# Kernel optimization log

Hardware: AMD Instinct MI355X
Metric: run time of the kernel (lower is better)

Reference implementation:

```python
import jax, jax.numpy as jnp
import numpy as np
import math

B, T, C, H = 8, 1024, 1024, 16
HS = C // H  # head size 64
FF = 4 * C
EPS = 1e-5


def quant_weight(W, e, b):
    """Fake-quant with straight-through rounding, per QLinear.forward.
    W:[...,out,in], e:[...,out,1], b:[...,out,1] -> effective weight 2**e * round_ste(clip(2**-e * W))."""
    b_rel = jax.nn.relu(b)
    mn = jnp.where(b_rel > 0, -(2.0 ** (b_rel - 1)), 0.0)
    mx = jnp.where(b_rel > 0, 2.0 ** (b_rel - 1) - 1.0, 0.0)
    qw = jnp.clip((2.0 ** (-e)) * W, mn, mx)
    w = qw + jax.lax.stop_gradient(jnp.round(qw) - qw)  # STE round
    return (2.0 ** e) * w


def layer_norm(x, g, beta):
    mu = jnp.mean(x, axis=-1, keepdims=True)
    var = jnp.mean((x - mu) ** 2, axis=-1, keepdims=True)
    return (x - mu) * jax.lax.rsqrt(var + EPS) * g + beta


def _uniform(key, shape, fan_in):
    s = 1.0 / math.sqrt(fan_in)
    return jax.random.uniform(key, shape, jnp.float32, -s, s)


def setup_inputs() -> dict:
    key = jax.random.key(0)
    ks = jax.random.split(key, 8)
    d = {"x": jax.random.normal(ks[0], (B, T, C), jnp.float32)}
    # stacked per-head QKV QLinear params (bias=False)
    d["Wq"] = _uniform(ks[1], (H, HS, C), C)
    d["Wk"] = _uniform(ks[2], (H, HS, C), C)
    d["Wv"] = _uniform(ks[3], (H, HS, C), C)
    for n in ("q", "k", "v"):
        d["e" + n] = jnp.full((H, HS, 1), -8.0, jnp.float32)
        d["b" + n] = jnp.full((H, HS, 1), 32.0, jnp.float32)
    # output projection QLinear (bias=True)
    d["Wp"] = _uniform(ks[4], (C, C), C)
    d["ep"] = jnp.full((C, 1), -8.0, jnp.float32)
    d["bp"] = jnp.full((C, 1), 32.0, jnp.float32)
    d["biasp"] = jnp.zeros((C,), jnp.float32)
    # FFN QLinears
    d["W1"] = _uniform(ks[5], (FF, C), C)
    d["e1"] = jnp.full((FF, 1), -8.0, jnp.float32)
    d["b1"] = jnp.full((FF, 1), 32.0, jnp.float32)
    d["bias1"] = jnp.zeros((FF,), jnp.float32)
    d["W2"] = _uniform(ks[6], (C, FF), FF)
    d["e2"] = jnp.full((C, 1), -8.0, jnp.float32)
    d["b2"] = jnp.full((C, 1), 32.0, jnp.float32)
    d["bias2"] = jnp.zeros((C,), jnp.float32)
    # LayerNorms
    d["g1"] = jnp.ones((C,), jnp.float32)
    d["be1"] = jnp.zeros((C,), jnp.float32)
    d["g2"] = jnp.ones((C,), jnp.float32)
    d["be2"] = jnp.zeros((C,), jnp.float32)
    return d


def block_forward(x, Wq, eq, bq, Wk, ek, bk, Wv, ev, bv,
                  Wp, ep, bp, biasp, W1, e1, b1, bias1, W2, e2, b2, bias2,
                  g1, be1, g2, be2):
    h = layer_norm(x, g1, be1)
    q = jnp.einsum('btc,hdc->bhtd', h, quant_weight(Wq, eq, bq))
    k = jnp.einsum('btc,hdc->bhtd', h, quant_weight(Wk, ek, bk))
    v = jnp.einsum('btc,hdc->bhtd', h, quant_weight(Wv, ev, bv))
    # NOTE: source scales by C**-0.5 where C = n_embd (not head_size)
    wei = jnp.einsum('bhtd,bhsd->bhts', q, k) * (C ** -0.5)
    causal = jnp.tril(jnp.ones((T, T), bool))
    wei = jnp.where(causal, wei, -jnp.inf)
    wei = jax.nn.softmax(wei, axis=-1)
    att = jnp.einsum('bhts,bhsd->bhtd', wei, v)  # [B,H,T,HS]
    att = att.transpose(0, 2, 1, 3).reshape(B, T, C)  # concat heads
    x = x + att @ quant_weight(Wp, ep, bp).T + biasp
    h2 = layer_norm(x, g2, be2)
    f = jax.nn.relu(h2 @ quant_weight(W1, e1, b1).T + bias1)
    f = f @ quant_weight(W2, e2, b2).T + bias2
    return x + f


def reference(x, Wq, eq, bq, Wk, ek, bk, Wv, ev, bv,
              Wp, ep, bp, biasp, W1, e1, b1, bias1, W2, e2, b2, bias2,
              g1, be1, g2, be2):
    return block_forward(x, Wq, eq, bq, Wk, ek, bk, Wv, ev, bv,
                         Wp, ep, bp, biasp, W1, e1, b1, bias1, W2, e2, b2, bias2,
                         g1, be1, g2, be2)
```

## Files before the change

kernel.cpp:

```cpp
#include <hip/hip_runtime.h>
#include <hip/hip_bf16.h>
#include <math.h>

#define DEVI __device__ __forceinline__

typedef __attribute__((ext_vector_type(8))) short bf16x8;
typedef __attribute__((ext_vector_type(4))) float f32x4;

DEVI unsigned short f2bf(float f) {
    union { float f; unsigned u; } v; v.f = f;
    unsigned r = v.u + 0x7FFFu + ((v.u >> 16) & 1u);
    return (unsigned short)(r >> 16);
}

DEVI void gload16(const void* g, void* l) {
    __builtin_amdgcn_global_load_lds((const __attribute__((address_space(1))) void*)g,
                                     (__attribute__((address_space(3))) void*)l, 16, 0, 0);
}

#define WAITVM8() asm volatile("s_waitcnt vmcnt(8)" ::: "memory")
#define WAITVM4() asm volatile("s_waitcnt vmcnt(4)" ::: "memory")
#define WAITVM0() asm volatile("s_waitcnt vmcnt(0)" ::: "memory")
#define WAITLG0() asm volatile("s_waitcnt lgkmcnt(0)" ::: "memory")
#define WAITLG8() asm volatile("s_waitcnt lgkmcnt(8)" ::: "memory")
#define BAR()     __builtin_amdgcn_s_barrier()
#define SB()      __builtin_amdgcn_sched_barrier(0)

__global__ __launch_bounds__(256) void quant6_kernel(
    const float* __restrict__ Wq, const float* __restrict__ Wk, const float* __restrict__ Wv,
    const float* __restrict__ Wp, const float* __restrict__ W1, const float* __restrict__ W2,
    const float* __restrict__ eq, const float* __restrict__ ek, const float* __restrict__ ev,
    const float* __restrict__ ep, const float* __restrict__ e1, const float* __restrict__ e2,
    const float* __restrict__ bq, const float* __restrict__ bk, const float* __restrict__ bv,
    const float* __restrict__ bp, const float* __restrict__ b1, const float* __restrict__ b2,
    unsigned short* __restrict__ Wqkvq, unsigned short* __restrict__ Wpq,
    unsigned short* __restrict__ W1q, unsigned short* __restrict__ W2q)
{
    const int M1 = 1 << 20;
    const int NCH = 3 * M1;
    for (int c = blockIdx.x * blockDim.x + threadIdx.x; c < NCH; c += gridDim.x * blockDim.x) {
        int elem = c * 4;
        const float *W, *e, *b; unsigned short* o; int lgK, local;
        if (elem < M1)            { W = Wq; e = eq; b = bq; o = Wqkvq;          lgK = 10; local = elem; }
        else if (elem < 2 * M1)   { W = Wk; e = ek; b = bk; o = Wqkvq + M1;     lgK = 10; local = elem - M1; }
        else if (elem < 3 * M1)   { W = Wv; e = ev; b = bv; o = Wqkvq + 2 * M1; lgK = 10; local = elem - 2 * M1; }
        else if (elem < 4 * M1)   { W = Wp; e = ep; b = bp; o = Wpq;            lgK = 10; local = elem - 3 * M1; }
        else if (elem < 8 * M1)   { W = W1; e = e1; b = b1; o = W1q;            lgK = 10; local = elem - 4 * M1; }
        else                      { W = W2; e = e2; b = b2; o = W2q;            lgK = 12; local = elem - 8 * M1; }
        int row = local >> lgK;
        float evv = e[row], bvv = b[row];
        float br = fmaxf(bvv, 0.f);
        float mn, mx;
        if (br > 0.f) { float p = exp2f(br - 1.f); mn = -p; mx = p - 1.f; }
        else          { mn = 0.f; mx = 0.f; }
        float si = exp2f(-evv), so = exp2f(evv);
        union { float4 v4; float a[4]; } v;
        v.v4 = *(const float4*)(W + local);
        union { unsigned short u[4]; unsigned long long ll; } ot;
        #pragma unroll
        for (int j = 0; j < 4; j++) {
            float qw = fminf(fmaxf(si * v.a[j], mn), mx);
            ot.u[j] = f2bf(so * rintf(qw));
        }
        *(unsigned long long*)(o + local) = ot.ll;
    }
}

__global__ __launch_bounds__(256) void ln_kernel(
    const float* __restrict__ x, const float* __restrict__ g, const float* __restrict__ be,
    unsigned short* __restrict__ out)
{
    int row = blockIdx.x;
    union { float4 v4; float a[4]; } v;
    v.v4 = ((const float4*)(x + (size_t)row * 1024))[threadIdx.x];
    float s = v.a[0] + v.a[1] + v.a[2] + v.a[3];
    float s2 = v.a[0]*v.a[0] + v.a[1]*v.a[1] + v.a[2]*v.a[2] + v.a[3]*v.a[3];
    #pragma unroll
    for (int off = 32; off > 0; off >>= 1) { s += __shfl_down(s, off); s2 += __shfl_down(s2, off); }
    __shared__ float ps[4], ps2[4];
    int wave = threadIdx.x >> 6, lane = threadIdx.x & 63;
    if (lane == 0) { ps[wave] = s; ps2[wave] = s2; }
    __syncthreads();
    float mu = (ps[0] + ps[1] + ps[2] + ps[3]) * (1.0f / 1024.0f);
    float var = (ps2[0] + ps2[1] + ps2[2] + ps2[3]) * (1.0f / 1024.0f) - mu * mu;
    float rs = rsqrtf(var + 1e-5f);
    int c = threadIdx.x * 4;
    union { unsigned short u[4]; unsigned long long ll; } o;
    #pragma unroll
    for (int j = 0; j < 4; j++) o.u[j] = f2bf((v.a[j] - mu) * rs * g[c + j] + be[c + j]);
    *(unsigned long long*)(out + (size_t)row * 1024 + c) = o.ll;
}

#define GSTAGE(buf, kt) do { \
    _Pragma("unroll") for (int q_ = 0; q_ < 4; q_++) { \
        int idx_ = q_ * 256 + tid; int row_ = idx_ >> 3; int gs_ = (idx_ & 7) ^ (row_ & 7); \
        gload16(A  + (size_t)(brow + row_) * K + (kt) * 64 + gs_ * 8, &As[buf][idx_ * 8]); \
        gload16(Bw + (size_t)(bcol + row_) * K + (kt) * 64 + gs_ * 8, &Bs[buf][idx_ * 8]); \
    } } while (0)

template<int EP>
__global__ __launch_bounds__(256) void gemm_bt(
    const unsigned short* __restrict__ A, const unsigned short* __restrict__ Bw,
    int N, int K,
    const float* __restrict__ bias, const float* __restrict__ res,
    float* __restrict__ outf, unsigned short* __restrict__ outb)
{
    __shared__ __align__(16) unsigned short As[2][128 * 64];
    __shared__ __align__(16) unsigned short Bs[2][128 * 64];
    int tid = threadIdx.x, lane = tid & 63, wave = tid >> 6;
    int gx = gridDim.x;
    int nwg = gx * gridDim.y;
    int id = blockIdx.y * gx + blockIdx.x;
    int swz = (id & 7) * (nwg >> 3) + (id >> 3);
    int brow = (swz / gx) * 128, bcol = (swz % gx) * 128;
    int wr = wave >> 1, wc = wave & 1;
    int r = lane & 15, g4 = lane >> 4;
    f32x4 acc[4][4];
    #pragma unroll
    for (int i = 0; i < 4; i++)
        #pragma unroll
        for (int j = 0; j < 4; j++) acc[i][j] = (f32x4){0.f, 0.f, 0.f, 0.f};

    int nt = K >> 6;
    GSTAGE(0, 0);
    __syncthreads();
    int cur = 0;
    for (int t = 0; t < nt; ++t) {
        if (t + 1 < nt) { GSTAGE(cur ^ 1, t + 1); WAITVM8(); }
        else            { WAITVM0(); }
        __builtin_amdgcn_s_barrier();
        #pragma unroll
        for (int kk = 0; kk < 2; kk++) {
            bf16x8 af[4], bfr[4];
            #pragma unroll
            for (int mi = 0; mi < 4; mi++) {
                int rh = wr * 64 + mi * 16 + r;
                af[mi] = *(const bf16x8*)&As[cur][rh * 64 + (((kk * 4 + g4) ^ (rh & 7)) << 3)];
            }
            #pragma unroll
            for (int ni = 0; ni < 4; ni++) {
                int rh = wc * 64 + ni * 16 + r;
                bfr[ni] = *(const bf16x8*)&Bs[cur][rh * 64 + (((kk * 4 + g4) ^ (rh & 7)) << 3)];
            }
            #pragma unroll
            for (int mi = 0; mi < 4; mi++)
                #pragma unroll
                for (int ni = 0; ni < 4; ni++)
                    acc[mi][ni] = __builtin_amdgcn_mfma_f32_16x16x32_bf16(af[mi], bfr[ni], acc[mi][ni], 0, 0, 0);
        }
        __builtin_amdgcn_s_barrier();
        cur ^= 1;
    }

    #pragma unroll
    for (int mi = 0; mi < 4; mi++)
        #pragma unroll
        for (int ni = 0; ni < 4; ni++)
            #pragma unroll
            for (int i = 0; i < 4; i++) {
                int row = brow + wr * 64 + mi * 16 + g4 * 4 + i;
                int col = bcol + wc * 64 + ni * 16 + r;
                float v = acc[mi][ni][i];
                if (EP == 0) {
                    outb[(size_t)row * N + col] = f2bf(v);
                } else if (EP == 1) {
                    outf[(size_t)row * N + col] = v + bias[col] + res[(size_t)row * N + col];
                } else {
                    outb[(size_t)row * N + col] = f2bf(fmaxf(v + bias[col], 0.f));
                }
            }
}

#define STAGE_A(b, h, kt) do { \
    _Pragma("unroll") \
    for (int ld = 0; ld < 2; ld++) { \
        int idx = ld * 512 + tid; int rw = idx >> 3; int gs = (idx & 7) ^ (rw & 7); \
        gload16(Aa + (size_t)(brow + (h) * 128 + rw) * K + (kt) * 64 + gs * 8, &As[b][h][idx * 8]); \
    } } while (0)

#define STAGE_B(b, h, kt) do { \
    _Pragma("unroll") \
    for (int ld = 0; ld < 2; ld++) { \
        int idx = ld * 512 + tid; int rw = idx >> 3; int gs = (idx & 7) ^ (rw & 7); \
        gload16(Bw + (size_t)(bcol + (h) * 128 + rw) * K + (kt) * 64 + gs * 8, &Bs[b][h][idx * 8]); \
    } } while (0)

#define RD_A(b, mh) do { \
    _Pragma("unroll") for (int mi = 0; mi < 4; mi++) \
    _Pragma("unroll") for (int kk = 0; kk < 2; kk++) { \
        int rh = (mh) * 64 + mi * 16 + r; \
        af[mi][kk] = *(const bf16x8*)&As[b][wr][rh * 64 + (((kk * 4 + g4) ^ (rh & 7)) << 3)]; \
    } } while (0)

#define RD_B2(b, nh) do { \
    _Pragma("unroll") for (int nj = 0; nj < 2; nj++) \
    _Pragma("unroll") for (int kk = 0; kk < 2; kk++) { \
        int rh = (wc & 1) * 64 + ((nh) * 2 + nj) * 16 + r; \
        bfr[(nh) * 2 + nj][kk] = *(const bf16x8*)&Bs[b][wc >> 1][rh * 64 + (((kk * 4 + g4) ^ (rh & 7)) << 3)]; \
    } } while (0)

#define QUAD(mh, nh) do { \
    __builtin_amdgcn_s_setprio(1); \
    _Pragma("unroll") for (int mi = 0; mi < 4; mi++) \
    _Pragma("unroll") for (int nj = 0; nj < 2; nj++) \
    _Pragma("unroll") for (int kk = 0; kk < 2; kk++) \
        acc[(mh) * 4 + mi][(nh) * 2 + nj] = __builtin_amdgcn_mfma_f32_16x16x32_bf16( \
            af[mi][kk], bfr[(nh) * 2 + nj][kk], acc[(mh) * 4 + mi][(nh) * 2 + nj], 0, 0, 0); \
    __builtin_amdgcn_s_setprio(0); \
    } while (0)

template<int EP>
__global__ __launch_bounds__(512, 2) void gemm256(
    const unsigned short* __restrict__ Aa, const unsigned short* __restrict__ Bw,
    int N, int K,
    const float* __restrict__ bias, const float* __restrict__ res,
    float* __restrict__ outf, unsigned short* __restrict__ outb)
{
    __shared__ __align__(16) unsigned short As[2][2][128 * 64];
    __shared__ __align__(16) unsigned short Bs[2][2][128 * 64];
    int tid = threadIdx.x, lane = tid & 63, wave = tid >> 6;
    int gx = gridDim.x;
    int nwg = gx * gridDim.y;
    int id = blockIdx.y * gx + blockIdx.x;
    int swz = (id & 7) * (nwg >> 3) + (id >> 3);
    int brow = (swz / gx) * 256, bcol = (swz % gx) * 256;
    int wr = wave >> 2, wc = wave & 3;
    int r = lane & 15, g4 = lane >> 4;
    int KT = K >> 6;

    f32x4 acc[8][4];
    #pragma unroll
    for (int i = 0; i < 8; i++)
        #pragma unroll
        for (int j = 0; j < 4; j++) acc[i][j] = (f32x4){0.f, 0.f, 0.f, 0.f};
    bf16x8 af[4][2], bfr[4][2];

    STAGE_A(0, 0, 0); STAGE_A(0, 1, 0); STAGE_B(0, 0, 0); STAGE_B(0, 1, 0);
    STAGE_B(1, 0, 1); STAGE_B(1, 1, 1);
    WAITVM4();
    BAR();

    for (int t = 0; t < KT; t += 2) {
        RD_A(0, 0); RD_B2(0, 0);
        STAGE_A(1, 0, t + 1);
        WAITLG8();
        BAR(); WAITLG0(); SB();
        QUAD(0, 0);
        BAR();
        RD_B2(0, 1);
        STAGE_A(1, 1, t + 1);
        BAR(); WAITLG0(); SB();
        QUAD(0, 1);
        BAR();
        RD_A(0, 1);
        if (t + 2 < KT) STAGE_B(0, 0, t + 2);
        BAR(); WAITLG0(); SB();
        QUAD(1, 1);
        BAR();
        if (t + 2 < KT) { STAGE_B(0, 1, t + 2); WAITVM4(); } else { WAITVM0(); }
        BAR(); WAITLG0(); SB();
        QUAD(1, 0);
        BAR();
        RD_A(1, 0); RD_B2(1, 0);
        if (t + 2 < KT) STAGE_A(0, 0, t + 2);
        WAITLG8();
        BAR(); WAITLG0(); SB();
        QUAD(0, 0);
        BAR();
        RD_B2(1, 1);
        if (t + 2 < KT) STAGE_A(0, 1, t + 2);
        BAR(); WAITLG0(); SB();
        QUAD(0, 1);
        BAR();
        RD_A(1, 1);
        if (t + 3 < KT) STAGE_B(1, 0, t + 3);
        BAR(); WAITLG0(); SB();
        QUAD(1, 1);
        BAR();
        if (t + 3 < KT) { STAGE_B(1, 1, t + 3); WAITVM4(); } else { WAITVM0(); }
        BAR(); WAITLG0(); SB();
        QUAD(1, 0);
        BAR();
    }

    #pragma unroll
    for (int m = 0; m < 8; m++)
        #pragma unroll
        for (int n = 0; n < 4; n++)
            #pragma unroll
            for (int j = 0; j < 4; j++) {
                int row = brow + wr * 128 + m * 16 + g4 * 4 + j;
                int col = bcol + wc * 64 + n * 16 + r;
                float v = acc[m][n][j];
                if (EP == 0) {
                    outb[(size_t)row * N + col] = f2bf(v);
                } else if (EP == 1) {
                    outf[(size_t)row * N + col] = v + bias[col] + res[(size_t)row * N + col];
                } else {
                    outb[(size_t)row * N + col] = f2bf(fmaxf(v + bias[col], 0.f));
                }
            }
}

__global__ __launch_bounds__(256) void attn_kernel(
    const unsigned short* __restrict__ qkv, unsigned short* __restrict__ att)
{
    __shared__ __align__(16) unsigned short Ks[2][64 * 64];
    __shared__ __align__(16) unsigned short Vt[2][64 * 64];
    __shared__ __align__(16) unsigned short Ps[64 * 64];
    int tid = threadIdx.x, lane = tid & 63, wave = tid >> 6;
    int pi = blockIdx.x;
    int bh = blockIdx.y, bb = bh >> 4, hh = bh & 15;
    int r = lane & 15, g4 = lane >> 4;
    const unsigned short* base = qkv + (size_t)bb * 1024 * 3072;
    const float SCL = 0.03125f * 1.4426950408889634f;
    int vd = tid & 63, vsb = tid >> 6;
    int prow = wave * 16 + r;
    int pswz = (r & 7) << 3;

    #pragma unroll
    for (int sub = 0; sub < 2; sub++) {
        int qi = sub ? (15 - pi) : pi;
        int q0 = qi * 64;
        int qrow = q0 + prow;

        bf16x8 qf[2];
        #pragma unroll
        for (int kk = 0; kk < 2; kk++)
            qf[kk] = *(const bf16x8*)&base[(size_t)qrow * 3072 + hh * 64 + kk * 32 + g4 * 8];

        f32x4 oacc[4];
        #pragma unroll
        for (int i = 0; i < 4; i++) oacc[i] = (f32x4){0.f, 0.f, 0.f, 0.f};
        float m_i = -INFINITY, l_i = 0.f;

        unsigned short vtmp[16];
        {
            #pragma unroll
            for (int half = 0; half < 2; half++) {
                int idx = half * 256 + tid;
                int row = idx >> 3, slot = idx & 7;
                int gs = slot ^ (row & 7);
                gload16(base + (size_t)row * 3072 + 1024 + hh * 64 + gs * 8, &Ks[0][idx * 8]);
            }
            #pragma unroll
            for (int i2 = 0; i2 < 16; i2++)
                vtmp[i2] = base[(size_t)(vsb * 16 + i2) * 3072 + 2048 + hh * 64 + vd];
            union { unsigned short u[8]; bf16x8 v; } w0, w1;
            #pragma unroll
            for (int i2 = 0; i2 < 8; i2++) { w0.u[i2] = vtmp[i2]; w1.u[i2] = vtmp[8 + i2]; }
            int s0 = (vsb * 2) ^ (vd & 7), s1 = (vsb * 2 + 1) ^ (vd & 7);
            *(bf16x8*)&Vt[0][vd * 64 + s0 * 8] = w0.v;
            *(bf16x8*)&Vt[0][vd * 64 + s1 * 8] = w1.v;
        }
        __syncthreads();

        for (int ki = 0; ki <= qi; ki++) {
            int cur = ki & 1;
            bool pre = (ki < qi);
            if (pre) {
                int k1 = (ki + 1) * 64;
                #pragma unroll
                for (int half = 0; half < 2; half++) {
                    int idx = half * 256 + tid;
                    int row = idx >> 3, slot = idx & 7;
                    int gs = slot ^ (row & 7);
                    gload16(base + (size_t)(k1 + row) * 3072 + 1024 + hh * 64 + gs * 8, &Ks[cur ^ 1][idx * 8]);
                }
                #pragma unroll
                for (int i2 = 0; i2 < 16; i2++)
                    vtmp[i2] = base[(size_t)(k1 + vsb * 16 + i2) * 3072 + 2048 + hh * 64 + vd];
            }

            int k0 = ki * 64;
            f32x4 sacc[4];
            #pragma unroll
            for (int c4 = 0; c4 < 4; c4++) sacc[c4] = (f32x4){0.f, 0.f, 0.f, 0.f};
            #pragma unroll
            for (int c4 = 0; c4 < 4; c4++) {
                int krow = c4 * 16 + r;
                #pragma unroll
                for (int kk = 0; kk < 2; kk++) {
                    int slot = (g4 + kk * 4) ^ (krow & 7);
                    bf16x8 kf = *(const bf16x8*)&Ks[cur][krow * 64 + slot * 8];
                    sacc[c4] = __builtin_amdgcn_mfma_f32_16x16x32_bf16(kf, qf[kk], sacc[c4], 0, 0, 0);
                }
            }
            bool diag = (ki == qi);
            float sv[4][4];
            float smax = -INFINITY;
            #pragma unroll
            for (int c4 = 0; c4 < 4; c4++)
                #pragma unroll
                for (int i = 0; i < 4; i++) {
                    float s = sacc[c4][i];
                    if (diag && (k0 + c4 * 16 + g4 * 4 + i) > qrow) s = -INFINITY;
                    sv[c4][i] = s;
                    smax = fmaxf(smax, s);
                }
            smax = fmaxf(smax, __shfl_xor(smax, 16));
            smax = fmaxf(smax, __shfl_xor(smax, 32));
            float mn = fmaxf(m_i, smax);
            float fs = exp2f((m_i - mn) * SCL);
            float nb = -mn * SCL;
            m_i = mn;
            float rsum = 0.f;
            float pv[4][4];
            #pragma unroll
            for (int c4 = 0; c4 < 4; c4++)
                #pragma unroll
                for (int i = 0; i < 4; i++) {
                    float p = exp2f(fmaf(sv[c4][i], SCL, nb));
                    pv[c4][i] = p;
                    rsum += p;
                }
            rsum += __shfl_xor(rsum, 16);
            rsum += __shfl_xor(rsum, 32);
            l_i = l_i * fs + rsum;
            #pragma unroll
            for (int n4 = 0; n4 < 4; n4++)
                #pragma unroll
                for (int i = 0; i < 4; i++) oacc[n4][i] *= fs;
            #pragma unroll
            for (int c4 = 0; c4 < 4; c4++) {
                union { unsigned short u[4]; unsigned long long ll; } pk;
                #pragma unroll
                for (int i = 0; i < 4; i++) pk.u[i] = f2bf(pv[c4][i]);
                int idx16 = (prow * 64 + c4 * 16 + g4 * 4) ^ pswz;
                *(unsigned long long*)&Ps[idx16] = pk.ll;
            }
            WAITLG0();
            if (pre) {
                union { unsigned short u[8]; bf16x8 v; } w0, w1;
                #pragma unroll
                for (int i2 = 0; i2 < 8; i2++) { w0.u[i2] = vtmp[i2]; w1.u[i2] = vtmp[8 + i2]; }
                int s0 = (vsb * 2) ^ (vd & 7), s1 = (vsb * 2 + 1) ^ (vd & 7);
                *(bf16x8*)&Vt[cur ^ 1][vd * 64 + s0 * 8] = w0.v;
                *(bf16x8*)&Vt[cur ^ 1][vd * 64 + s1 * 8] = w1.v;
            }
            bf16x8 pa[2];
            #pragma unroll
            for (int kk = 0; kk < 2; kk++)
                pa[kk] = *(const bf16x8*)&Ps[(prow * 64 + kk * 32 + g4 * 8) ^ pswz];
            #pragma unroll
            for (int n4 = 0; n4 < 4; n4++) {
                int d = n4 * 16 + r;
                #pragma unroll
                for (int kk = 0; kk < 2; kk++) {
                    bf16x8 vf = *(const bf16x8*)&Vt[cur][d * 64 + (((kk * 4 + g4) ^ (d & 7)) << 3)];
                    oacc[n4] = __builtin_amdgcn_mfma_f32_16x16x32_bf16(vf, pa[kk], oacc[n4], 0, 0, 0);
                }
            }
            __syncthreads();
        }

        float inv = 1.f / l_i;
        #pragma unroll
        for (int n4 = 0; n4 < 4; n4++) {
            union { unsigned short u[4]; unsigned long long ll; } ok;
            #pragma unroll
            for (int i = 0; i < 4; i++) ok.u[i] = f2bf(oacc[n4][i] * inv);
            size_t oidx = ((size_t)(bb * 1024 + qrow)) * 1024 + hh * 64 + n4 * 16 + g4 * 4;
            *(unsigned long long*)&att[oidx] = ok.ll;
        }
    }
}

extern "C" void kernel_launch(void* const* d_in, const int* in_sizes, int n_in,
                              void* d_out, int out_size, void* d_ws, size_t ws_size,
                              hipStream_t stream)
{
    const float* x     = (const float*)d_in[0];
    const float* Wq    = (const float*)d_in[1];
    const float* Wk    = (const float*)d_in[2];
    const float* Wv    = (const float*)d_in[3];
    const float* eq    = (const float*)d_in[4];
    const float* bq    = (const float*)d_in[5];
    const float* ek    = (const float*)d_in[6];
    const float* bk    = (const float*)d_in[7];
    const float* ev    = (const float*)d_in[8];
    const float* bv    = (const float*)d_in[9];
    const float* Wp    = (const float*)d_in[10];
    const float* ep    = (const float*)d_in[11];
    const float* bp    = (const float*)d_in[12];
    const float* biasp = (const float*)d_in[13];
    const float* W1    = (const float*)d_in[14];
    const float* e1    = (const float*)d_in[15];
    const float* b1    = (const float*)d_in[16];
    const float* bias1 = (const float*)d_in[17];
    const float* W2    = (const float*)d_in[18];
    const float* e2    = (const float*)d_in[19];
    const float* b2    = (const float*)d_in[20];
    const float* bias2 = (const float*)d_in[21];
    const float* g1    = (const float*)d_in[22];
    const float* be1   = (const float*)d_in[23];
    const float* g2    = (const float*)d_in[24];
    const float* be2   = (const float*)d_in[25];

    const size_t MB = 1ull << 20;
    char* ws = (char*)d_ws;
    unsigned short* Wqkvq = (unsigned short*)(ws);
    unsigned short* Wpq   = (unsigned short*)(ws + 6 * MB);
    unsigned short* W1q   = (unsigned short*)(ws + 8 * MB);
    unsigned short* W2q   = (unsigned short*)(ws + 16 * MB);
    unsigned short* hbuf  = (unsigned short*)(ws + 24 * MB);
    unsigned short* qkvb  = (unsigned short*)(ws + 40 * MB);
    unsigned short* fbuf  = qkvb;
    unsigned short* attb  = (unsigned short*)(ws + 88 * MB);
    float*          x2    = (float*)(ws + 104 * MB);

    quant6_kernel<<<2048, 256, 0, stream>>>(Wq, Wk, Wv, Wp, W1, W2,
                                            eq, ek, ev, ep, e1, e2,
                                            bq, bk, bv, bp, b1, b2,
                                            Wqkvq, Wpq, W1q, W2q);

    ln_kernel<<<8192, 256, 0, stream>>>(x, g1, be1, hbuf);
    gemm256<0><<<dim3(12, 32), 512, 0, stream>>>(hbuf, Wqkvq, 3072, 1024, nullptr, nullptr, nullptr, qkvb);
    attn_kernel<<<dim3(8, 128), 256, 0, stream>>>(qkvb, attb);
    gemm_bt<1><<<dim3(8, 64), 256, 0, stream>>>(attb, Wpq, 1024, 1024, biasp, x, x2, nullptr);
    ln_kernel<<<8192, 256, 0, stream>>>(x2, g2, be2, hbuf);
    gemm256<2><<<dim3(16, 32), 512, 0, stream>>>(hbuf, W1q, 4096, 1024, bias1, nullptr, nullptr, fbuf);
    gemm_bt<1><<<dim3(8, 64), 256, 0, stream>>>(fbuf, W2q, 1024, 4096, bias2, x2, (float*)d_out, nullptr);
}
```

Baseline: 349.5 us.

## Share K/V tiles across two query tiles per 512-thread attention block

The attention kernel now uses 512 threads, and each half of the block handles an adjacent query tile. Every K/V tile loaded into shared memory serves both query tiles, which halves global K/V traffic and staging per block. It also adds lazy online-softmax rescaling that only rescales when the row max grows by more than a threshold, packed bf16 conversion through v_cvt_pk_bf16_f32, and padding of the V-transpose LDS rows to a stride of 66. The costs are that the lower-tile waves sit idle on the last diagonal tile, and that the padded stride leaves 16-byte LDS accesses that are not 16-byte aligned.

```diff
diff --git a/kernel.cpp b/kernel.cpp
--- a/kernel.cpp
+++ b/kernel.cpp
@@ -11,6 +11,12 @@
     union { float f; unsigned u; } v; v.f = f;
     unsigned r = v.u + 0x7FFFu + ((v.u >> 16) & 1u);
     return (unsigned short)(r >> 16);
+}
+
+DEVI unsigned cvtpk(float lo, float hi) {
+    unsigned d;
+    asm volatile("v_cvt_pk_bf16_f32 %0, %1, %2" : "=v"(d) : "v"(lo), "v"(hi));
+    return d;
 }
 
 DEVI void gload16(const void* g, void* l) {
@@ -302,27 +308,28 @@
             }
 }
 
-__global__ __launch_bounds__(256) void attn_kernel(
+__global__ __launch_bounds__(512, 4) void attn_kernel(
     const unsigned short* __restrict__ qkv, unsigned short* __restrict__ att)
 {
     __shared__ __align__(16) unsigned short Ks[2][64 * 64];
-    __shared__ __align__(16) unsigned short Vt[2][64 * 64];
-    __shared__ __align__(16) unsigned short Ps[64 * 64];
-    int tid = threadIdx.x, lane = tid & 63, wave = tid >> 6;
+    __shared__ __align__(16) unsigned short Vt[2][64 * 66];
+    __shared__ __align__(16) unsigned short Ps[2][64 * 64];
+    int tid = threadIdx.x, lane = tid & 63, w = tid >> 6;
+    int half = w >> 2;
     int pi = blockIdx.x;
     int bh = blockIdx.y, bb = bh >> 4, hh = bh & 15;
     int r = lane & 15, g4 = lane >> 4;
     const unsigned short* base = qkv + (size_t)bb * 1024 * 3072;
     const float SCL = 0.03125f * 1.4426950408889634f;
     int vd = tid & 63, vsb = tid >> 6;
-    int prow = wave * 16 + r;
+    int prow = (w & 3) * 16 + r;
     int pswz = (r & 7) << 3;
 
-    #pragma unroll
-    for (int sub = 0; sub < 2; sub++) {
-        int qi = sub ? (15 - pi) : pi;
-        int q0 = qi * 64;
-        int qrow = q0 + prow;
+    for (int sidx = 0; sidx < 2; sidx++) {
+        int s = sidx ? (7 - pi) : pi;
+        int qt = 2 * s + half;
+        int qtmax = 2 * s + 1;
+        int qrow = qt * 64 + prow;
 
         bf16x8 qf[2];
         #pragma unroll
@@ -334,121 +341,115 @@
         for (int i = 0; i < 4; i++) oacc[i] = (f32x4){0.f, 0.f, 0.f, 0.f};
         float m_i = -INFINITY, l_i = 0.f;
 
-        unsigned short vtmp[16];
+        unsigned short vtmp[8];
         {
-            #pragma unroll
-            for (int half = 0; half < 2; half++) {
-                int idx = half * 256 + tid;
-                int row = idx >> 3, slot = idx & 7;
-                int gs = slot ^ (row & 7);
-                gload16(base + (size_t)row * 3072 + 1024 + hh * 64 + gs * 8, &Ks[0][idx * 8]);
-            }
-            #pragma unroll
-            for (int i2 = 0; i2 < 16; i2++)
-                vtmp[i2] = base[(size_t)(vsb * 16 + i2) * 3072 + 2048 + hh * 64 + vd];
-            union { unsigned short u[8]; bf16x8 v; } w0, w1;
-            #pragma unroll
-            for (int i2 = 0; i2 < 8; i2++) { w0.u[i2] = vtmp[i2]; w1.u[i2] = vtmp[8 + i2]; }
-            int s0 = (vsb * 2) ^ (vd & 7), s1 = (vsb * 2 + 1) ^ (vd & 7);
-            *(bf16x8*)&Vt[0][vd * 64 + s0 * 8] = w0.v;
-            *(bf16x8*)&Vt[0][vd * 64 + s1 * 8] = w1.v;
+            int row = tid >> 3, slot = tid & 7;
+            int gs = slot ^ (row & 7);
+            gload16(base + (size_t)row * 3072 + 1024 + hh * 64 + gs * 8, &Ks[0][tid * 8]);
+            #pragma unroll
+            for (int i2 = 0; i2 < 8; i2++)
+                vtmp[i2] = base[(size_t)(vsb * 8 + i2) * 3072 + 2048 + hh * 64 + vd];
+            union { unsigned short u[8]; bf16x8 v; } w0;
+            #pragma unroll
+            for (int i2 = 0; i2 < 8; i2++) w0.u[i2] = vtmp[i2];
+            *(bf16x8*)&Vt[0][vd * 66 + (vsb ^ (vd & 7)) * 8] = w0.v;
         }
         __syncthreads();
 
-        for (int ki = 0; ki <= qi; ki++) {
+        for (int ki = 0; ki <= qtmax; ki++) {
             int cur = ki & 1;
-            bool pre = (ki < qi);
+            bool pre = (ki < qtmax);
+            bool act = (ki <= qt);
             if (pre) {
                 int k1 = (ki + 1) * 64;
-                #pragma unroll
-                for (int half = 0; half < 2; half++) {
-                    int idx = half * 256 + tid;
-                    int row = idx >> 3, slot = idx & 7;
-                    int gs = slot ^ (row & 7);
-                    gload16(base + (size_t)(k1 + row) * 3072 + 1024 + hh * 64 + gs * 8, &Ks[cur ^ 1][idx * 8]);
+                int row = tid >> 3, slot = tid & 7;
+                int gs = slot ^ (row & 7);
+                gload16(base + (size_t)(k1 + row) * 3072 + 1024 + hh * 64 + gs * 8, &Ks[cur ^ 1][tid * 8]);
+                #pragma unroll
+                for (int i2 = 0; i2 < 8; i2++)
+                    vtmp[i2] = base[(size_t)(k1 + vsb * 8 + i2) * 3072 + 2048 + hh * 64 + vd];
+            }
+
+            if (act) {
+                int k0 = ki * 64;
+                f32x4 sacc[4];
+                #pragma unroll
+                for (int c4 = 0; c4 < 4; c4++) sacc[c4] = (f32x4){0.f, 0.f, 0.f, 0.f};
+                #pragma unroll
+                for (int c4 = 0; c4 < 4; c4++) {
+                    int krow = c4 * 16 + r;
+                    #pragma unroll
+                    for (int kk = 0; kk < 2; kk++) {
+                        int slot = (g4 + kk * 4) ^ (krow & 7);
+                        bf16x8 kf = *(const bf16x8*)&Ks[cur][krow * 64 + slot * 8];
+                        sacc[c4] = __builtin_amdgcn_mfma_f32_16x16x32_bf16(kf, qf[kk], sacc[c4], 0, 0, 0);
+                    }
                 }
-                #pragma unroll
-                for (int i2 = 0; i2 < 16; i2++)
-                    vtmp[i2] = base[(size_t)(k1 + vsb * 16 + i2) * 3072 + 2048 + hh * 64 + vd];
-            }
-
-            int k0 = ki * 64;
-            f32x4 sacc[4];
-            #pragma unroll
-            for (int c4 = 0; c4 < 4; c4++) sacc[c4] = (f32x4){0.f, 0.f, 0.f, 0.f};
-            #pragma unroll
-            for (int c4 = 0; c4 < 4; c4++) {
-                int krow = c4 * 16 + r;
-                #pragma unroll
-                for (int kk = 0; kk < 2; kk++) {
-                    int slot = (g4 + kk * 4) ^ (krow & 7);
-                    bf16x8 kf = *(const bf16x8*)&Ks[cur][krow * 64 + slot * 8];
-                    sacc[c4] = __builtin_amdgcn_mfma_f32_16x16x32_bf16(kf, qf[kk], sacc[c4], 0, 0, 0);
+                bool diag = (ki == qt);
+                float sv[4][4];
+                float smax = -INFINITY;
+                #pragma unroll
+                for (int c4 = 0; c4 < 4; c4++)
+                    #pragma unroll
+                    for (int i = 0; i < 4; i++) {
+                        float sa = sacc[c4][i];
+                        if (diag && (k0 + c4 * 16 + g4 * 4 + i) > qrow) sa = -INFINITY;
+                        sv[c4][i] = sa;
+                        smax = fmaxf(smax, sa);
+                    }
+                smax = fmaxf(smax, __shfl_xor(smax, 16));
+                smax = fmaxf(smax, __shfl_xor(smax, 32));
+                if (!__all((smax - m_i) * SCL <= 8.f)) {
+                    float mn = fmaxf(m_i, smax);
+                    float fs = exp2f((m_i - mn) * SCL);
+                    m_i = mn;
+                    l_i *= fs;
+                    #pragma unroll
+                    for (int n4 = 0; n4 < 4; n4++)
+                        #pragma unroll
+                        for (int i = 0; i < 4; i++) oacc[n4][i] *= fs;
                 }
-            }
-            bool diag = (ki == qi);
-            float sv[4][4];
-            float smax = -INFINITY;
-            #pragma unroll
-            for (int c4 = 0; c4 < 4; c4++)
-                #pragma unroll
-                for (int i = 0; i < 4; i++) {
-                    float s = sacc[c4][i];
-                    if (diag && (k0 + c4 * 16 + g4 * 4 + i) > qrow) s = -INFINITY;
-                    sv[c4][i] = s;
-                    smax = fmaxf(smax, s);
+                float nb = -m_i * SCL;
+                float rsum = 0.f;
+                float pv[4][4];
+                #pragma unroll
+                for (int c4 = 0; c4 < 4; c4++)
+                    #pragma unroll
+                    for (int i = 0; i < 4; i++) {
+                        float p = exp2f(fmaf(sv[c4][i], SCL, nb));
+                        pv[c4][i] = p;
+                        rsum += p;
+                    }
+                rsum += __shfl_xor(rsum, 16);
+                rsum += __shfl_xor(rsum, 32);
+                l_i += rsum;
+                #pragma unroll
+                for (int c4 = 0; c4 < 4; c4++) {
+                    unsigned long long ll = (unsigned long long)cvtpk(pv[c4][0], pv[c4][1])
+                                          | ((unsigned long long)cvtpk(pv[c4][2], pv[c4][3]) << 32);
+                    *(unsigned long long*)&Ps[half][(prow * 64 + c4 * 16 + g4 * 4) ^ pswz] = ll;
                 }
-            smax = fmaxf(smax, __shfl_xor(smax, 16));
-            smax = fmaxf(smax, __shfl_xor(smax, 32));
-            float mn = fmaxf(m_i, smax);
-            float fs = exp2f((m_i - mn) * SCL);
-            float nb = -mn * SCL;
-            m_i = mn;
-            float rsum = 0.f;
-            float pv[4][4];
-            #pragma unroll
-            for (int c4 = 0; c4 < 4; c4++)
-                #pragma unroll
-                for (int i = 0; i < 4; i++) {
-                    float p = exp2f(fmaf(sv[c4][i], SCL, nb));
-                    pv[c4][i] = p;
-                    rsum += p;
-                }
-            rsum += __shfl_xor(rsum, 16);
-            rsum += __shfl_xor(rsum, 32);
-            l_i = l_i * fs + rsum;
-            #pragma unroll
-            for (int n4 = 0; n4 < 4; n4++)
-                #pragma unroll
-                for (int i = 0; i < 4; i++) oacc[n4][i] *= fs;
-            #pragma unroll
-            for (int c4 = 0; c4 < 4; c4++) {
-                union { unsigned short u[4]; unsigned long long ll; } pk;
-                #pragma unroll
-                for (int i = 0; i < 4; i++) pk.u[i] = f2bf(pv[c4][i]);
-                int idx16 = (prow * 64 + c4 * 16 + g4 * 4) ^ pswz;
-                *(unsigned long long*)&Ps[idx16] = pk.ll;
-            }
-            WAITLG0();
+                WAITLG0();
+            }
             if (pre) {
-                union { unsigned short u[8]; bf16x8 v; } w0, w1;
-                #pragma unroll
-                for (int i2 = 0; i2 < 8; i2++) { w0.u[i2] = vtmp[i2]; w1.u[i2] = vtmp[8 + i2]; }
-                int s0 = (vsb * 2) ^ (vd & 7), s1 = (vsb * 2 + 1) ^ (vd & 7);
-                *(bf16x8*)&Vt[cur ^ 1][vd * 64 + s0 * 8] = w0.v;
-                *(bf16x8*)&Vt[cur ^ 1][vd * 64 + s1 * 8] = w1.v;
-            }
-            bf16x8 pa[2];
-            #pragma unroll
-            for (int kk = 0; kk < 2; kk++)
-                pa[kk] = *(const bf16x8*)&Ps[(prow * 64 + kk * 32 + g4 * 8) ^ pswz];
-            #pragma unroll
-            for (int n4 = 0; n4 < 4; n4++) {
-                int d = n4 * 16 + r;
-                #pragma unroll
-                for (int kk = 0; kk < 2; kk++) {
-                    bf16x8 vf = *(const bf16x8*)&Vt[cur][d * 64 + (((kk * 4 + g4) ^ (d & 7)) << 3)];
-                    oacc[n4] = __builtin_amdgcn_mfma_f32_16x16x32_bf16(vf, pa[kk], oacc[n4], 0, 0, 0);
+                union { unsigned short u[8]; bf16x8 v; } w0;
+                #pragma unroll
+                for (int i2 = 0; i2 < 8; i2++) w0.u[i2] = vtmp[i2];
+                *(bf16x8*)&Vt[cur ^ 1][vd * 66 + (vsb ^ (vd & 7)) * 8] = w0.v;
+            }
+            if (act) {
+                bf16x8 pa[2];
+                #pragma unroll
+                for (int kk = 0; kk < 2; kk++)
+                    pa[kk] = *(const bf16x8*)&Ps[half][(prow * 64 + kk * 32 + g4 * 8) ^ pswz];
+                #pragma unroll
+                for (int n4 = 0; n4 < 4; n4++) {
+                    int d = n4 * 16 + r;
+                    #pragma unroll
+                    for (int kk = 0; kk < 2; kk++) {
+                        bf16x8 vf = *(const bf16x8*)&Vt[cur][d * 66 + (((kk * 4 + g4) ^ (d & 7)) << 3)];
+                        oacc[n4] = __builtin_amdgcn_mfma_f32_16x16x32_bf16(vf, pa[kk], oacc[n4], 0, 0, 0);
+                    }
                 }
             }
             __syncthreads();
@@ -457,11 +458,10 @@
         float inv = 1.f / l_i;
         #pragma unroll
         for (int n4 = 0; n4 < 4; n4++) {
-            union { unsigned short u[4]; unsigned long long ll; } ok;
-            #pragma unroll
-            for (int i = 0; i < 4; i++) ok.u[i] = f2bf(oacc[n4][i] * inv);
+            unsigned long long ll = (unsigned long long)cvtpk(oacc[n4][0] * inv, oacc[n4][1] * inv)
+                                  | ((unsigned long long)cvtpk(oacc[n4][2] * inv, oacc[n4][3] * inv) << 32);
             size_t oidx = ((size_t)(bb * 1024 + qrow)) * 1024 + hh * 64 + n4 * 16 + g4 * 4;
-            *(unsigned long long*)&att[oidx] = ok.ll;
+            *(unsigned long long*)&att[oidx] = ll;
         }
     }
 }
@@ -516,7 +516,7 @@
 
     ln_kernel<<<8192, 256, 0, stream>>>(x, g1, be1, hbuf);
     gemm256<0><<<dim3(12, 32), 512, 0, stream>>>(hbuf, Wqkvq, 3072, 1024, nullptr, nullptr, nullptr, qkvb);
-    attn_kernel<<<dim3(8, 128), 256, 0, stream>>>(qkvb, attb);
+    attn_kernel<<<dim3(4, 128), 512, 0, stream>>>(qkvb, attb);
     gemm_bt<1><<<dim3(8, 64), 256, 0, stream>>>(attb, Wpq, 1024, 1024, biasp, x, x2, nullptr);
     ln_kernel<<<8192, 256, 0, stream>>>(x2, g2, be2, hbuf);
     gemm256<2><<<dim3(16, 32), 512, 0, stream>>>(hbuf, W1q, 4096, 1024, bias1, nullptr, nullptr, fbuf);
```

After: 329.1 us. 1.06x faster.
